# Kernel tuning notes

Hardware: AMD Instinct MI355X
Metric: run time of the kernel (lower is better)

## Reference

```python
import jax, jax.numpy as jnp
import numpy as np

N = 100000   # nodes
D = 128      # embedding_dim
E = 1600000  # edges (avg in-degree 16)
L = 2        # num_layers
CURV = 1.0   # positive curvature (repo default -1.0 is NaN under sqrt)


def mobius_addition(x, y, c):
    xy = jnp.sum(x * y, axis=-1, keepdims=True)
    xn = jnp.sum(x * x, axis=-1, keepdims=True)
    yn = jnp.sum(y * y, axis=-1, keepdims=True)
    num = (1 + 2 * c * xy + c * yn) * x + (1 - c * xn) * y
    den = 1 + 2 * c * xy + c * c * xn * yn
    return num / den


def exp_map(x, v, c):
    vn = jnp.linalg.norm(v, axis=-1, keepdims=True)
    sc = jnp.sqrt(c)
    second = jnp.tanh(sc * vn / 2) * v / (sc * vn)
    return mobius_addition(x, second, c)


def log_map(x, y, c):
    add = mobius_addition(-x, y, c)
    an = jnp.linalg.norm(add, axis=-1, keepdims=True)
    sc = jnp.sqrt(c)
    return (2 / sc) * jnp.arctanh(sc * an) * add / an


def setup_inputs() -> dict:
    key = jax.random.key(0)
    ks = jax.random.split(key, 10)
    s = 1.0 / np.sqrt(D)  # torch Linear init scale
    embeddings = 0.01 * jax.random.normal(ks[0], (N, D), dtype=jnp.float32)  # ||x||<1 keeps atanh finite
    Wq = jax.random.uniform(ks[1], (L, D, D), jnp.float32, -s, s)
    bq = jax.random.uniform(ks[2], (L, D), jnp.float32, -s, s)
    Wk = jax.random.uniform(ks[3], (L, D, D), jnp.float32, -s, s)
    bk = jax.random.uniform(ks[4], (L, D), jnp.float32, -s, s)
    Wv = jax.random.uniform(ks[5], (L, D, D), jnp.float32, -s, s)
    bv = jax.random.uniform(ks[6], (L, D), jnp.float32, -s, s)
    src = jax.random.randint(ks[7], (E,), 0, N, dtype=jnp.int32)
    # guarantee every node has >=1 in-edge (DGL would leave isolated nodes at h=0 -> exp_map NaN)
    dst = jnp.concatenate([jnp.arange(N, dtype=jnp.int32),
                           jax.random.randint(ks[8], (E - N,), 0, N, dtype=jnp.int32)])
    curvature = jnp.array([CURV], dtype=jnp.float32)
    return {"embeddings": embeddings, "Wq": Wq, "bq": bq, "Wk": Wk, "bk": bk,
            "Wv": Wv, "bv": bv, "curvature": curvature, "src": src, "dst": dst}


def reference(embeddings, Wq, bq, Wk, bk, Wv, bv, curvature, src, dst):
    c = curvature  # shape [1], broadcasts against [..., 1]
    scale = float(D) ** 0.5
    x = embeddings
    origin = jnp.zeros((1, D), dtype=x.dtype)
    for l in range(Wq.shape[0]):
        t = log_map(origin, x, c)                      # [N, D] tangent at origin
        q = t @ Wq[l].T + bq[l]
        k = t @ Wk[l].T + bk[l]
        v = t @ Wv[l].T + bv[l]
        e = jnp.sum(k[src] * q[dst], axis=-1) / scale  # [E] edge scores
        m = jax.ops.segment_max(e, dst, num_segments=N)
        p = jnp.exp(e - m[dst])
        z = jax.ops.segment_sum(p, dst, num_segments=N)
        alpha = p / z[dst]                             # segment softmax over in-edges
        h = jax.ops.segment_sum(alpha[:, None] * v[src], dst, num_segments=N)
        x = exp_map(origin, h, c)
    return x
```

## Files before the change

kernel.cpp:

```cpp
#include <hip/hip_runtime.h>
#include <hip/hip_bf16.h>
#include <stdint.h>

typedef __attribute__((ext_vector_type(8))) short short8;
typedef __attribute__((ext_vector_type(4))) float f32x4;
typedef __attribute__((ext_vector_type(2))) float f32x2;
typedef __attribute__((ext_vector_type(4))) unsigned int u32x4;
typedef __attribute__((ext_vector_type(2))) _Float16 half2_t;

__device__ __forceinline__ uint32_t pack2(float a, float b) {
    auto r = __builtin_amdgcn_cvt_pkrtz(a, b);
    return __builtin_bit_cast(uint32_t, r);
}
__device__ __forceinline__ uint16_t f2h(float x) {
    auto r = __builtin_amdgcn_cvt_pkrtz(x, 0.0f);
    return (uint16_t)(__builtin_bit_cast(uint32_t, r) & 0xffffu);
}

__device__ __forceinline__ void agg_hist_add(int b, int lane, int* lcnt) {
    int prev = __shfl_up(b, 1);
    bool head = (lane == 0) || (b != prev);
    unsigned long long heads = __ballot(head);
    unsigned long long mask_le = ((1ull << lane) << 1) - 1ull;
    unsigned long long g = heads & ~mask_le;
    int nexthead = g ? (int)__builtin_ctzll(g) : 64;
    if (head && b >= 0) atomicAdd(&lcnt[b], nexthead - lane);
}
__device__ __forceinline__ int agg_slot(int b, int lane, int* lcnt) {
    int prev = __shfl_up(b, 1);
    bool head = (lane == 0) || (b != prev);
    unsigned long long heads = __ballot(head);
    unsigned long long mask_le = ((1ull << lane) << 1) - 1ull;
    unsigned long long m = heads & mask_le;
    int myhead = 63 - (int)__builtin_clzll(m);
    unsigned long long g = heads & ~mask_le;
    int nexthead = g ? (int)__builtin_ctzll(g) : 64;
    int base = 0;
    if (lane == myhead && b >= 0) base = atomicAdd(&lcnt[b], nexthead - lane);
    base = __shfl(base, myhead);
    return base + (lane - myhead);
}

#define DIM 128
#define BKT_SHIFT 7
#define BKT_NODES 128
#define MAX_BKT 1024
#define BIN_TILE 16384
#define CSR_CAP 3072
#define LDS_W_STRIDE 136
#define NW_BLK 16

__global__ __launch_bounds__(256) void prep_kernel(
    const int* __restrict__ dst, int* __restrict__ bucket_cnt, int E, int nbuckets, int nbin,
    const float* __restrict__ Wq, const float* __restrict__ Wk, const float* __restrict__ Wv,
    uint16_t* __restrict__ w_h, int wtotal,
    const float* __restrict__ x, uint16_t* __restrict__ t, const float* __restrict__ curv,
    int N) {
    __shared__ int lcnt[MAX_BKT];
    int bx = blockIdx.x;
    if (bx < nbin) {
        for (int i = threadIdx.x; i < nbuckets; i += 256) lcnt[i] = 0;
        __syncthreads();
        int base = bx * BIN_TILE;
        int end = min(base + BIN_TILE, E);
        int lane = threadIdx.x & 63;
        for (int e0 = base; e0 < end; e0 += 256) {
            int e = e0 + threadIdx.x;
            int b = (e < end) ? (dst[e] >> BKT_SHIFT) : -1;
            agg_hist_add(b, lane, lcnt);
        }
        __syncthreads();
        for (int i = threadIdx.x; i < nbuckets; i += 256)
            if (lcnt[i]) atomicAdd(&bucket_cnt[i], lcnt[i]);
    } else if (bx < nbin + NW_BLK) {
        int per_l = 3 * DIM * DIM;
        for (int i = (bx - nbin) * 256 + threadIdx.x; i < wtotal; i += 256 * NW_BLK) {
            int l = i / per_l;
            int rem = i % per_l;
            int mat = rem / (DIM * DIM);
            int idx = rem % (DIM * DIM);
            const float* s = (mat == 0) ? Wq : (mat == 1) ? Wk : Wv;
            w_h[i] = f2h(s[l * DIM * DIM + idx]);
        }
    } else {
        int tid = threadIdx.x;
        int n = (bx - nbin - NW_BLK) * 32 + (tid >> 3);
        if (n >= N) return;
        int ln8 = tid & 7;
        const float4* xp = (const float4*)(x + (size_t)n * DIM) + ln8 * 4;
        float4 a0 = xp[0], a1 = xp[1], a2 = xp[2], a3 = xp[3];
        float ss = a0.x * a0.x + a0.y * a0.y + a0.z * a0.z + a0.w * a0.w
                 + a1.x * a1.x + a1.y * a1.y + a1.z * a1.z + a1.w * a1.w
                 + a2.x * a2.x + a2.y * a2.y + a2.z * a2.z + a2.w * a2.w
                 + a3.x * a3.x + a3.y * a3.y + a3.z * a3.z + a3.w * a3.w;
        #pragma unroll
        for (int off = 4; off >= 1; off >>= 1) ss += __shfl_xor(ss, off);
        float c = curv[0];
        float sc = sqrtf(c);
        float r = sqrtf(ss);
        float z = sc * r;
        float f = (r > 1e-30f) ? __logf((1.0f + z) / (1.0f - z)) / (sc * r) : 2.0f;
        uint4 o0, o1;
        o0.x = pack2(f * a0.x, f * a0.y); o0.y = pack2(f * a0.z, f * a0.w);
        o0.z = pack2(f * a1.x, f * a1.y); o0.w = pack2(f * a1.z, f * a1.w);
        o1.x = pack2(f * a2.x, f * a2.y); o1.y = pack2(f * a2.z, f * a2.w);
        o1.z = pack2(f * a3.x, f * a3.y); o1.w = pack2(f * a3.z, f * a3.w);
        uint4* tp = (uint4*)(t + (size_t)n * DIM) + ln8 * 2;
        tp[0] = o0; tp[1] = o1;
    }
}

__global__ __launch_bounds__(256) void bscan_kernel(const int* __restrict__ bucket_cnt,
                                                    int* __restrict__ bstart,
                                                    int* __restrict__ bcursor,
                                                    int nbuckets, int E) {
    __shared__ int lds[256];
    int tid = threadIdx.x;
    int v[4];
    #pragma unroll
    for (int c = 0; c < 4; c++) {
        int idx = c * 256 + tid;
        v[c] = (idx < nbuckets) ? bucket_cnt[idx] : 0;
    }
    int run = 0;
    #pragma unroll
    for (int c = 0; c < 4; c++) {
        lds[tid] = v[c]; __syncthreads();
        for (int off = 1; off < 256; off <<= 1) {
            int t = (tid >= off) ? lds[tid - off] : 0;
            __syncthreads();
            lds[tid] += t;
            __syncthreads();
        }
        int ex = run + lds[tid] - v[c];
        int idx = c * 256 + tid;
        if (idx < nbuckets) { bstart[idx] = ex; bcursor[idx] = ex; }
        run += lds[255];
        __syncthreads();
    }
    if (tid == 0) bstart[nbuckets] = E;
}

__global__ __launch_bounds__(256) void bin_kernel(const int* __restrict__ src,
                                                  const int* __restrict__ dst,
                                                  int* __restrict__ bcursor,
                                                  int2* __restrict__ pair_buf,
                                                  int E, int nbuckets) {
    __shared__ int lcnt[MAX_BKT];
    __shared__ int lbase[MAX_BKT];
    int lane = threadIdx.x & 63;
    for (int i = threadIdx.x; i < nbuckets; i += 256) lcnt[i] = 0;
    __syncthreads();
    int base = blockIdx.x * BIN_TILE;
    int end = min(base + BIN_TILE, E);
    for (int e0 = base; e0 < end; e0 += 256) {
        int e = e0 + threadIdx.x;
        int b = (e < end) ? (dst[e] >> BKT_SHIFT) : -1;
        agg_hist_add(b, lane, lcnt);
    }
    __syncthreads();
    for (int i = threadIdx.x; i < nbuckets; i += 256) {
        int c = lcnt[i];
        lbase[i] = c ? atomicAdd(&bcursor[i], c) : 0;
    }
    __syncthreads();
    for (int i = threadIdx.x; i < nbuckets; i += 256) lcnt[i] = 0;
    __syncthreads();
    for (int e0 = base; e0 < end; e0 += 256) {
        int e = e0 + threadIdx.x;
        bool valid = (e < end);
        int d = valid ? dst[e] : 0;
        int b = valid ? (d >> BKT_SHIFT) : -1;
        int slot = agg_slot(b, lane, lcnt);
        if (valid) pair_buf[(size_t)lbase[b] + slot] = make_int2(src[e], d);
    }
}

__global__ __launch_bounds__(256) void csr_kernel(const int2* __restrict__ pair_buf,
                                                  const int* __restrict__ bstart,
                                                  int* __restrict__ row_start,
                                                  int* __restrict__ esrc,
                                                  int N, int E) {
    __shared__ int cnt[BKT_NODES], incl[BKT_NODES], cur[BKT_NODES];
    __shared__ int lsrc[CSR_CAP];
    int b = blockIdx.x;
    int node0 = b << BKT_SHIFT;
    int p0 = bstart[b], p1 = bstart[b + 1];
    int cntb = p1 - p0;
    int tid = threadIdx.x;
    if (tid < BKT_NODES) { cnt[tid] = 0; cur[tid] = 0; }
    __syncthreads();
    for (int i = p0 + tid; i < p1; i += 256)
        atomicAdd(&cnt[pair_buf[i].y & (BKT_NODES - 1)], 1);
    __syncthreads();
    if (tid < BKT_NODES) incl[tid] = cnt[tid];
    __syncthreads();
    for (int off = 1; off < BKT_NODES; off <<= 1) {
        int v = 0;
        if (tid < BKT_NODES && tid >= off) v = incl[tid - off];
        __syncthreads();
        if (tid < BKT_NODES) incl[tid] += v;
        __syncthreads();
    }
    if (tid < BKT_NODES) {
        int n = node0 + tid;
        if (n < N) row_start[n] = p0 + incl[tid] - cnt[tid];
    }
    if (b == 0 && tid == 0) row_start[N] = E;
    bool fit = (cntb <= CSR_CAP);
    __syncthreads();
    for (int i = p0 + tid; i < p1; i += 256) {
        int2 pr = pair_buf[i];
        int ln = pr.y & (BKT_NODES - 1);
        int slot = incl[ln] - cnt[ln] + atomicAdd(&cur[ln], 1);
        if (fit) lsrc[slot] = pr.x;
        else     esrc[p0 + slot] = pr.x;
    }
    __syncthreads();
    if (fit)
        for (int i = tid; i < cntb; i += 256) esrc[p0 + i] = lsrc[i];
}

__global__ __launch_bounds__(256) void qkv_gemm_kernel(
    const uint16_t* __restrict__ t,
    const uint16_t* __restrict__ w,
    const float* __restrict__ bq, const float* __restrict__ bk, const float* __restrict__ bv,
    uint16_t* __restrict__ qout, uint8_t* __restrict__ k8out, uint16_t* __restrict__ vout,
    int N) {
    __shared__ uint16_t lw[DIM * LDS_W_STRIDE];
    int mat = blockIdx.y;
    const uint16_t* wm = w + (size_t)mat * DIM * DIM;
    {
        int r = threadIdx.x >> 1, hf = (threadIdx.x & 1) * 64;
        const uint4* srcp = (const uint4*)(wm + r * DIM + hf);
        uint4* dstp = (uint4*)(lw + r * LDS_W_STRIDE + hf);
        #pragma unroll
        for (int i = 0; i < 8; i++) dstp[i] = srcp[i];
    }
    __syncthreads();
    int wave = threadIdx.x >> 6, lane = threadIdx.x & 63;
    int sub = lane & 15, quad = lane >> 4;
    int node0 = blockIdx.x * 256 + wave * 64;
    const float* bias = (mat == 0) ? bq : (mat == 1) ? bk : bv;
    f32x4 acc[8][4] = {};
    #pragma unroll
    for (int k0 = 0; k0 < DIM; k0 += 32) {
        short8 b[4];
        #pragma unroll
        for (int g = 0; g < 4; g++) {
            int node = node0 + g * 16 + sub;
            int nodec = (node < N) ? node : (N - 1);
            b[g] = *(const short8*)(t + (size_t)nodec * DIM + k0 + quad * 8);
        }
        short8 a[8];
        #pragma unroll
        for (int tile = 0; tile < 8; tile++)
            a[tile] = *(const short8*)(lw + (tile * 16 + sub) * LDS_W_STRIDE + k0 + quad * 8);
        #pragma unroll
        for (int tile = 0; tile < 8; tile++)
            #pragma unroll
            for (int g = 0; g < 4; g++)
                acc[tile][g] = __builtin_amdgcn_mfma_f32_16x16x32_f16(a[tile], b[g], acc[tile][g], 0, 0, 0);
    }
    #pragma unroll
    for (int g = 0; g < 4; g++) {
        int node = node0 + g * 16 + sub;
        if (node >= N) continue;
        if (mat == 1) {
            #pragma unroll
            for (int tile = 0; tile < 8; tile++) {
                float4 bs = *(const float4*)(bias + tile * 16 + quad * 4);
                int pk = 0;
                pk = __builtin_amdgcn_cvt_pk_fp8_f32(acc[tile][g][0] + bs.x, acc[tile][g][1] + bs.y, pk, false);
                pk = __builtin_amdgcn_cvt_pk_fp8_f32(acc[tile][g][2] + bs.z, acc[tile][g][3] + bs.w, pk, true);
                *(uint32_t*)(k8out + (size_t)node * DIM + tile * 16 + quad * 4) = (uint32_t)pk;
            }
        } else {
            uint16_t* outp = (mat == 0) ? qout : vout;
            #pragma unroll
            for (int tile = 0; tile < 8; tile++) {
                float4 bs = *(const float4*)(bias + tile * 16 + quad * 4);
                uint2 pk;
                pk.x = pack2(acc[tile][g][0] + bs.x, acc[tile][g][1] + bs.y);
                pk.y = pack2(acc[tile][g][2] + bs.z, acc[tile][g][3] + bs.w);
                *(uint2*)(outp + (size_t)node * DIM + tile * 16 + quad * 4) = pk;
            }
        }
    }
}

__global__ __launch_bounds__(256) void attn_kernel(
    const uint16_t* __restrict__ q, const uint8_t* __restrict__ k8,
    const uint16_t* __restrict__ v,
    const int* __restrict__ row_start, const int* __restrict__ esrc,
    const float* __restrict__ curv,
    uint16_t* __restrict__ t_out,
    float* __restrict__ x_out,
    int N, int mode) {
    int wave = threadIdx.x >> 6, lane = threadIdx.x & 63;
    int sub = lane & 15, quad = lane >> 4;
    int n = blockIdx.x * 4 + wave;
    if (n >= N) return;
    int s0 = row_start[n], s1 = row_start[n + 1];
    u32x4 qu = __builtin_nontemporal_load((const u32x4*)(q + (size_t)n * DIM + sub * 8));
    f32x2 qf2[4];
    #pragma unroll
    for (int i = 0; i < 4; i++) {
        half2_t qh = __builtin_bit_cast(half2_t, qu[i]);
        qf2[i][0] = (float)qh.x; qf2[i][1] = (float)qh.y;
    }
    const float K2 = 0.12751744154470514f;
    float l = 0.0f;
    float h[8] = {0, 0, 0, 0, 0, 0, 0, 0};
    for (int s = s0; s < s1; s += 64) {
        int idx = s + lane;
        int sidx_all = __builtin_nontemporal_load(esrc + (idx < s1 ? idx : s1 - 1));
        int m = min(16, ((s1 - s) + 3) >> 2);
        for (int it0 = 0; it0 < m; it0 += 4) {
            uint2 ku[4]; uint4 vu[4];
            #pragma unroll
            for (int u = 0; u < 4; u++) {
                int sx = __shfl(sidx_all, (it0 + u) * 4 + quad);
                int ko = sx * DIM + sub * 8;
                ku[u] = *(const uint2*)(k8 + ko);
                vu[u] = *(const uint4*)(v + ko);
            }
            #pragma unroll
            for (int u = 0; u < 4; u++) {
                int e = s + (it0 + u) * 4 + quad;
                bool valid = (e < s1);
                f32x2 d0 = __builtin_amdgcn_cvt_pk_f32_fp8(ku[u].x, false);
                f32x2 d1 = __builtin_amdgcn_cvt_pk_f32_fp8(ku[u].x, true);
                f32x2 d2 = __builtin_amdgcn_cvt_pk_f32_fp8(ku[u].y, false);
                f32x2 d3 = __builtin_amdgcn_cvt_pk_f32_fp8(ku[u].y, true);
                f32x2 acc2 = qf2[0] * d0;
                acc2 += qf2[1] * d1;
                acc2 += qf2[2] * d2;
                acc2 += qf2[3] * d3;
                float dot = acc2[0] + acc2[1];
                #pragma unroll
                for (int off = 8; off >= 1; off >>= 1) dot += __shfl_xor(dot, off);
                float p = valid ? __builtin_amdgcn_exp2f(dot * K2) : 0.0f;
                l += p;
                #pragma unroll
                for (int i = 0; i < 4; i++) {
                    half2_t vh = __builtin_bit_cast(half2_t, ((const uint32_t*)&vu[u])[i]);
                    h[2 * i]     = fmaf(p, (float)vh.x, h[2 * i]);
                    h[2 * i + 1] = fmaf(p, (float)vh.y, h[2 * i + 1]);
                }
            }
        }
    }
    #pragma unroll
    for (int off = 16; off <= 32; off <<= 1) {
        l += __shfl_xor(l, off);
        #pragma unroll
        for (int j = 0; j < 8; j++) h[j] += __shfl_xor(h[j], off);
    }
    float rl = 1.0f / l;
    #pragma unroll
    for (int j = 0; j < 8; j++) h[j] *= rl;
    if (mode == 0) {
        if (quad == 0) {
            uint4 pk;
            pk.x = pack2(h[0], h[1]); pk.y = pack2(h[2], h[3]);
            pk.z = pack2(h[4], h[5]); pk.w = pack2(h[6], h[7]);
            *(uint4*)(t_out + (size_t)n * DIM + sub * 8) = pk;
        }
    } else {
        float ss = 0.0f;
        #pragma unroll
        for (int j = 0; j < 8; j++) ss += h[j] * h[j];
        #pragma unroll
        for (int off = 8; off >= 1; off >>= 1) ss += __shfl_xor(ss, off);
        float c = curv[0];
        float sc = sqrtf(c);
        float nh = sqrtf(ss);
        float f = (nh > 1e-30f) ? tanhf(sc * nh * 0.5f) / (sc * nh) : 0.5f;
        if (quad == 0) {
            f32x4 o0 = {f * h[0], f * h[1], f * h[2], f * h[3]};
            f32x4 o1 = {f * h[4], f * h[5], f * h[6], f * h[7]};
            __builtin_nontemporal_store(o0, (f32x4*)(x_out + (size_t)n * DIM + sub * 8));
            __builtin_nontemporal_store(o1, (f32x4*)(x_out + (size_t)n * DIM + sub * 8 + 4));
        }
    }
}

extern "C" void kernel_launch(void* const* d_in, const int* in_sizes, int n_in,
                              void* d_out, int out_size, void* d_ws, size_t ws_size,
                              hipStream_t stream) {
    const float* emb  = (const float*)d_in[0];
    const float* Wq   = (const float*)d_in[1];
    const float* bq   = (const float*)d_in[2];
    const float* Wk   = (const float*)d_in[3];
    const float* bk   = (const float*)d_in[4];
    const float* Wv   = (const float*)d_in[5];
    const float* bv   = (const float*)d_in[6];
    const float* curv = (const float*)d_in[7];
    const int*   srcp = (const int*)d_in[8];
    const int*   dstp = (const int*)d_in[9];

    const int N = in_sizes[0] / DIM;
    const int L = in_sizes[2] / DIM;
    const int E = in_sizes[8];

    uint8_t* ws = (uint8_t*)d_ws;
    size_t off = 0;
    auto carve = [&](size_t bytes) { size_t o = off; off = (off + bytes + 255) & ~(size_t)255; return o; };
    uint16_t* t_buf   = (uint16_t*)(ws + carve((size_t)N * DIM * 2));
    uint16_t* qb      = (uint16_t*)(ws + carve((size_t)N * DIM * 2));
    uint16_t* vb      = (uint16_t*)(ws + carve((size_t)N * DIM * 2));
    uint8_t*  k8b     = (uint8_t*)(ws + carve((size_t)N * DIM));
    uint16_t* w_h     = (uint16_t*)(ws + carve((size_t)L * 3 * DIM * DIM * 2));
    int* row_start    = (int*)(ws + carve((size_t)(N + 1) * 4));
    int* bucket_cnt   = (int*)(ws + carve(MAX_BKT * 4));
    int* bstart       = (int*)(ws + carve((MAX_BKT + 1) * 4));
    int* bcursor      = (int*)(ws + carve(MAX_BKT * 4));
    int* esrc         = (int*)(ws + carve((size_t)E * 4));
    (void)ws_size;
    int2* pair_buf = (int2*)qb;

    const int nbuckets = (N + BKT_NODES - 1) >> BKT_SHIFT;
    const int nbin = (E + BIN_TILE - 1) / BIN_TILE;
    const int wtotal = L * 3 * DIM * DIM;

    (void)hipMemsetAsync(bucket_cnt, 0, (size_t)nbuckets * 4, stream);
    int prep_grid = nbin + NW_BLK + (N + 31) / 32;
    prep_kernel<<<prep_grid, 256, 0, stream>>>(dstp, bucket_cnt, E, nbuckets, nbin,
                                               Wq, Wk, Wv, w_h, wtotal,
                                               emb, t_buf, curv, N);
    bscan_kernel<<<1, 256, 0, stream>>>(bucket_cnt, bstart, bcursor, nbuckets, E);
    bin_kernel<<<nbin, 256, 0, stream>>>(srcp, dstp, bcursor, pair_buf, E, nbuckets);
    csr_kernel<<<nbuckets, 256, 0, stream>>>(pair_buf, bstart, row_start, esrc, N, E);

    dim3 ggrid((N + 255) / 256, 3);
    for (int l = 0; l < L; l++) {
        qkv_gemm_kernel<<<ggrid, 256, 0, stream>>>(
            t_buf, w_h + (size_t)l * 3 * DIM * DIM,
            bq + (size_t)l * DIM, bk + (size_t)l * DIM, bv + (size_t)l * DIM,
            qb, k8b, vb, N);
        int mode = (l == L - 1) ? 1 : 0;
        attn_kernel<<<(N + 3) / 4, 256, 0, stream>>>(
            qb, k8b, vb, row_start, esrc, curv, t_buf, (float*)d_out, N, mode);
    }
}
```

Measured before the change: 505.4 us.

## Fuse bucket scan into prep via last-block, drop bin recount, use fp16 accumulation

The bucket prefix scan moves into the histogram blocks of prep_kernel. The last block to finish, found through an atomic done counter, performs the scan, which removes one kernel launch. bin_kernel no longer rebuilds a per-block histogram in LDS; it takes slots straight from global bcursor with wave-aggregated atomics, trading a second pass over dst for more global atomic contention. The attention accumulation changes from fp32 FMAs to packed half2 arithmetic, which halves ALU work and registers but risks precision loss and fp16 overflow in the weighted sums.

```diff
diff --git a/kernel.cpp b/kernel.cpp
--- a/kernel.cpp
+++ b/kernel.cpp
@@ -26,7 +26,7 @@
     int nexthead = g ? (int)__builtin_ctzll(g) : 64;
     if (head && b >= 0) atomicAdd(&lcnt[b], nexthead - lane);
 }
-__device__ __forceinline__ int agg_slot(int b, int lane, int* lcnt) {
+__device__ __forceinline__ int agg_slot(int b, int lane, int* cnt) {
     int prev = __shfl_up(b, 1);
     bool head = (lane == 0) || (b != prev);
     unsigned long long heads = __ballot(head);
@@ -36,7 +36,7 @@
     unsigned long long g = heads & ~mask_le;
     int nexthead = g ? (int)__builtin_ctzll(g) : 64;
     int base = 0;
-    if (lane == myhead && b >= 0) base = atomicAdd(&lcnt[b], nexthead - lane);
+    if (lane == myhead && b >= 0) base = atomicAdd(&cnt[b], nexthead - lane);
     base = __shfl(base, myhead);
     return base + (lane - myhead);
 }
@@ -51,30 +51,68 @@
 #define NW_BLK 16
 
 __global__ __launch_bounds__(256) void prep_kernel(
-    const int* __restrict__ dst, int* __restrict__ bucket_cnt, int E, int nbuckets, int nbin,
+    const int* __restrict__ dst, int* __restrict__ bucket_cnt, int* __restrict__ done_cnt,
+    int* __restrict__ bstart, int* __restrict__ bcursor,
+    int E, int nbuckets, int nbin,
     const float* __restrict__ Wq, const float* __restrict__ Wk, const float* __restrict__ Wv,
     uint16_t* __restrict__ w_h, int wtotal,
     const float* __restrict__ x, uint16_t* __restrict__ t, const float* __restrict__ curv,
     int N) {
     __shared__ int lcnt[MAX_BKT];
+    __shared__ int is_last;
     int bx = blockIdx.x;
+    int tid = threadIdx.x;
     if (bx < nbin) {
-        for (int i = threadIdx.x; i < nbuckets; i += 256) lcnt[i] = 0;
+        for (int i = tid; i < nbuckets; i += 256) lcnt[i] = 0;
         __syncthreads();
         int base = bx * BIN_TILE;
         int end = min(base + BIN_TILE, E);
-        int lane = threadIdx.x & 63;
+        int lane = tid & 63;
         for (int e0 = base; e0 < end; e0 += 256) {
-            int e = e0 + threadIdx.x;
+            int e = e0 + tid;
             int b = (e < end) ? (dst[e] >> BKT_SHIFT) : -1;
             agg_hist_add(b, lane, lcnt);
         }
         __syncthreads();
-        for (int i = threadIdx.x; i < nbuckets; i += 256)
+        for (int i = tid; i < nbuckets; i += 256)
             if (lcnt[i]) atomicAdd(&bucket_cnt[i], lcnt[i]);
+        if (tid == 0) {
+            __threadfence();
+            int d = atomicAdd(done_cnt, 1);
+            is_last = (d == nbin - 1);
+        }
+        __syncthreads();
+        if (is_last) {
+            __threadfence();
+            int v4[4];
+            #pragma unroll
+            for (int c = 0; c < 4; c++) {
+                int idx = c * 256 + tid;
+                v4[c] = (idx < nbuckets)
+                    ? __hip_atomic_load(&bucket_cnt[idx], __ATOMIC_RELAXED, __HIP_MEMORY_SCOPE_AGENT)
+                    : 0;
+            }
+            int run = 0;
+            #pragma unroll
+            for (int c = 0; c < 4; c++) {
+                lcnt[tid] = v4[c]; __syncthreads();
+                for (int off = 1; off < 256; off <<= 1) {
+                    int tv = (tid >= off) ? lcnt[tid - off] : 0;
+                    __syncthreads();
+                    lcnt[tid] += tv;
+                    __syncthreads();
+                }
+                int ex = run + lcnt[tid] - v4[c];
+                int idx = c * 256 + tid;
+                if (idx < nbuckets) { bstart[idx] = ex; bcursor[idx] = ex; }
+                run += lcnt[255];
+                __syncthreads();
+            }
+            if (tid == 0) bstart[nbuckets] = E;
+        }
     } else if (bx < nbin + NW_BLK) {
         int per_l = 3 * DIM * DIM;
-        for (int i = (bx - nbin) * 256 + threadIdx.x; i < wtotal; i += 256 * NW_BLK) {
+        for (int i = (bx - nbin) * 256 + tid; i < wtotal; i += 256 * NW_BLK) {
             int l = i / per_l;
             int rem = i % per_l;
             int mat = rem / (DIM * DIM);
@@ -83,7 +121,6 @@
             w_h[i] = f2h(s[l * DIM * DIM + idx]);
         }
     } else {
-        int tid = threadIdx.x;
         int n = (bx - nbin - NW_BLK) * 32 + (tid >> 3);
         if (n >= N) return;
         int ln8 = tid & 7;
@@ -110,69 +147,21 @@
     }
 }
 
-__global__ __launch_bounds__(256) void bscan_kernel(const int* __restrict__ bucket_cnt,
-                                                    int* __restrict__ bstart,
-                                                    int* __restrict__ bcursor,
-                                                    int nbuckets, int E) {
-    __shared__ int lds[256];
-    int tid = threadIdx.x;
-    int v[4];
-    #pragma unroll
-    for (int c = 0; c < 4; c++) {
-        int idx = c * 256 + tid;
-        v[c] = (idx < nbuckets) ? bucket_cnt[idx] : 0;
-    }
-    int run = 0;
-    #pragma unroll
-    for (int c = 0; c < 4; c++) {
-        lds[tid] = v[c]; __syncthreads();
-        for (int off = 1; off < 256; off <<= 1) {
-            int t = (tid >= off) ? lds[tid - off] : 0;
-            __syncthreads();
-            lds[tid] += t;
-            __syncthreads();
-        }
-        int ex = run + lds[tid] - v[c];
-        int idx = c * 256 + tid;
-        if (idx < nbuckets) { bstart[idx] = ex; bcursor[idx] = ex; }
-        run += lds[255];
-        __syncthreads();
-    }
-    if (tid == 0) bstart[nbuckets] = E;
-}
-
 __global__ __launch_bounds__(256) void bin_kernel(const int* __restrict__ src,
                                                   const int* __restrict__ dst,
                                                   int* __restrict__ bcursor,
                                                   int2* __restrict__ pair_buf,
-                                                  int E, int nbuckets) {
-    __shared__ int lcnt[MAX_BKT];
-    __shared__ int lbase[MAX_BKT];
+                                                  int E) {
     int lane = threadIdx.x & 63;
-    for (int i = threadIdx.x; i < nbuckets; i += 256) lcnt[i] = 0;
-    __syncthreads();
     int base = blockIdx.x * BIN_TILE;
     int end = min(base + BIN_TILE, E);
-    for (int e0 = base; e0 < end; e0 += 256) {
-        int e = e0 + threadIdx.x;
-        int b = (e < end) ? (dst[e] >> BKT_SHIFT) : -1;
-        agg_hist_add(b, lane, lcnt);
-    }
-    __syncthreads();
-    for (int i = threadIdx.x; i < nbuckets; i += 256) {
-        int c = lcnt[i];
-        lbase[i] = c ? atomicAdd(&bcursor[i], c) : 0;
-    }
-    __syncthreads();
-    for (int i = threadIdx.x; i < nbuckets; i += 256) lcnt[i] = 0;
-    __syncthreads();
     for (int e0 = base; e0 < end; e0 += 256) {
         int e = e0 + threadIdx.x;
         bool valid = (e < end);
         int d = valid ? dst[e] : 0;
         int b = valid ? (d >> BKT_SHIFT) : -1;
-        int slot = agg_slot(b, lane, lcnt);
-        if (valid) pair_buf[(size_t)lbase[b] + slot] = make_int2(src[e], d);
+        int slot = agg_slot(b, lane, bcursor);
+        if (valid) pair_buf[slot] = make_int2(src[e], d);
     }
 }
 
@@ -311,7 +300,7 @@
     }
     const float K2 = 0.12751744154470514f;
     float l = 0.0f;
-    float h[8] = {0, 0, 0, 0, 0, 0, 0, 0};
+    half2_t h2[4] = {};
     for (int s = s0; s < s1; s += 64) {
         int idx = s + lane;
         int sidx_all = __builtin_nontemporal_load(esrc + (idx < s1 ? idx : s1 - 1));
@@ -342,11 +331,12 @@
                 for (int off = 8; off >= 1; off >>= 1) dot += __shfl_xor(dot, off);
                 float p = valid ? __builtin_amdgcn_exp2f(dot * K2) : 0.0f;
                 l += p;
+                _Float16 pf = (_Float16)p;
+                half2_t ph = {pf, pf};
                 #pragma unroll
                 for (int i = 0; i < 4; i++) {
                     half2_t vh = __builtin_bit_cast(half2_t, ((const uint32_t*)&vu[u])[i]);
-                    h[2 * i]     = fmaf(p, (float)vh.x, h[2 * i]);
-                    h[2 * i + 1] = fmaf(p, (float)vh.y, h[2 * i + 1]);
+                    h2[i] += ph * vh;
                 }
             }
         }
@@ -355,19 +345,31 @@
     for (int off = 16; off <= 32; off <<= 1) {
         l += __shfl_xor(l, off);
         #pragma unroll
-        for (int j = 0; j < 8; j++) h[j] += __shfl_xor(h[j], off);
+        for (int i = 0; i < 4; i++) {
+            uint32_t hw = __builtin_bit_cast(uint32_t, h2[i]);
+            hw = __shfl_xor(hw, off);
+            h2[i] += __builtin_bit_cast(half2_t, hw);
+        }
     }
     float rl = 1.0f / l;
-    #pragma unroll
-    for (int j = 0; j < 8; j++) h[j] *= rl;
     if (mode == 0) {
         if (quad == 0) {
+            _Float16 rlh = (_Float16)rl;
+            half2_t rl2 = {rlh, rlh};
             uint4 pk;
-            pk.x = pack2(h[0], h[1]); pk.y = pack2(h[2], h[3]);
-            pk.z = pack2(h[4], h[5]); pk.w = pack2(h[6], h[7]);
+            pk.x = __builtin_bit_cast(uint32_t, h2[0] * rl2);
+            pk.y = __builtin_bit_cast(uint32_t, h2[1] * rl2);
+            pk.z = __builtin_bit_cast(uint32_t, h2[2] * rl2);
+            pk.w = __builtin_bit_cast(uint32_t, h2[3] * rl2);
             *(uint4*)(t_out + (size_t)n * DIM + sub * 8) = pk;
         }
     } else {
+        float h[8];
+        #pragma unroll
+        for (int i = 0; i < 4; i++) {
+            h[2 * i]     = (float)h2[i].x * rl;
+            h[2 * i + 1] = (float)h2[i].y * rl;
+        }
         float ss = 0.0f;
         #pragma unroll
         for (int j = 0; j < 8; j++) ss += h[j] * h[j];
@@ -413,24 +415,25 @@
     uint8_t*  k8b     = (uint8_t*)(ws + carve((size_t)N * DIM));
     uint16_t* w_h     = (uint16_t*)(ws + carve((size_t)L * 3 * DIM * DIM * 2));
     int* row_start    = (int*)(ws + carve((size_t)(N + 1) * 4));
-    int* bucket_cnt   = (int*)(ws + carve(MAX_BKT * 4));
+    int* bucket_cnt   = (int*)(ws + carve((MAX_BKT + 1) * 4));
     int* bstart       = (int*)(ws + carve((MAX_BKT + 1) * 4));
     int* bcursor      = (int*)(ws + carve(MAX_BKT * 4));
     int* esrc         = (int*)(ws + carve((size_t)E * 4));
     (void)ws_size;
+    int* done_cnt = bucket_cnt + MAX_BKT;
     int2* pair_buf = (int2*)qb;
 
     const int nbuckets = (N + BKT_NODES - 1) >> BKT_SHIFT;
     const int nbin = (E + BIN_TILE - 1) / BIN_TILE;
     const int wtotal = L * 3 * DIM * DIM;
 
-    (void)hipMemsetAsync(bucket_cnt, 0, (size_t)nbuckets * 4, stream);
+    (void)hipMemsetAsync(bucket_cnt, 0, (size_t)(MAX_BKT + 1) * 4, stream);
     int prep_grid = nbin + NW_BLK + (N + 31) / 32;
-    prep_kernel<<<prep_grid, 256, 0, stream>>>(dstp, bucket_cnt, E, nbuckets, nbin,
+    prep_kernel<<<prep_grid, 256, 0, stream>>>(dstp, bucket_cnt, done_cnt, bstart, bcursor,
+                                               E, nbuckets, nbin,
                                                Wq, Wk, Wv, w_h, wtotal,
                                                emb, t_buf, curv, N);
-    bscan_kernel<<<1, 256, 0, stream>>>(bucket_cnt, bstart, bcursor, nbuckets, E);
-    bin_kernel<<<nbin, 256, 0, stream>>>(srcp, dstp, bcursor, pair_buf, E, nbuckets);
+    bin_kernel<<<nbin, 256, 0, stream>>>(srcp, dstp, bcursor, pair_buf, E);
     csr_kernel<<<nbuckets, 256, 0, stream>>>(pair_buf, bstart, row_start, esrc, N, E);
 
     dim3 ggrid((N + 255) / 256, 3);
```

Measured after the change: 782.8 us. +54.9%, slower.
